# Kernel optimization log

Measured on AMD Instinct MI355X. Metric: run time of the kernel, lower is better.

## Reference

```python
import jax, jax.numpy as jnp
import numpy as np

N_EMBED = 1024
N_HEAD = 64  # head (value) dimension, per source: Linear(n_embed, n_head)
B = 8
C = 2048


def setup_inputs() -> dict:
    key = jax.random.key(0)
    k1, k2, k3, k4, k5 = jax.random.split(key, 5)
    bound = 1.0 / np.sqrt(N_EMBED)  # torch Linear default init range
    x = jax.random.normal(k1, (B, C, N_EMBED), dtype=jnp.float32)
    Wq = jax.random.uniform(k2, (N_EMBED, N_HEAD), dtype=jnp.float32, minval=-bound, maxval=bound)
    Wk = jax.random.uniform(k3, (N_EMBED, N_HEAD), dtype=jnp.float32, minval=-bound, maxval=bound)
    Wv = jax.random.uniform(k4, (N_EMBED, N_HEAD), dtype=jnp.float32, minval=-bound, maxval=bound)
    zero_mask = jax.random.randint(k5, (B, C), 0, 2) == 1
    return {"x": x, "Wq": Wq, "Wk": Wk, "Wv": Wv, "zero_mask": zero_mask}


def reference(x, Wq, Wk, Wv, zero_mask):
    # x: [B, C, n_embed]; zero_mask: [B, C] bool (zeroes whole query rows post-softmax)
    Bc, Cc, _ = x.shape
    q = x @ Wq  # [B, C, H]
    k = x @ Wk
    v = x @ Wv
    # NOTE: source scales by C**-0.5 (sequence length), not head_dim**-0.5
    scores = jnp.einsum('bqh,bkh->bqk', q, k) * (float(Cc) ** -0.5)  # [B, C, C]
    causal = jnp.tril(jnp.ones((Cc, Cc), dtype=bool))
    scores = jnp.where(causal[None], scores, -jnp.inf)
    a = jax.nn.softmax(scores, axis=-1)
    a = jnp.where(zero_mask[..., None], jnp.zeros((), dtype=a.dtype), a)  # post-softmax zero mask
    return a @ v  # [B, C, H]
```

## Files before the change

kernel.cpp:

```cpp
#include <hip/hip_runtime.h>
#include <math.h>


#define B_ 8
#define C_ 2048
#define E_ 1024
#define H_ 64
#define SCALE (0.02209708691207961f * 1.4426950408889634f)

typedef __attribute__((ext_vector_type(8))) short short8;
typedef __attribute__((ext_vector_type(4))) float floatx4;

union BF8 { short8 s8; unsigned int u[4]; };

static __device__ __forceinline__ unsigned int pack_bf2(float lo, float hi) {
    unsigned int a = __builtin_bit_cast(unsigned int, lo);
    unsigned int b = __builtin_bit_cast(unsigned int, hi);
    return (a >> 16) | (b & 0xFFFF0000u);
}
static __device__ __forceinline__ unsigned short f2bf(float f) {
    return (unsigned short)(__builtin_bit_cast(unsigned int, f) >> 16);
}
static __device__ __forceinline__ void load_lds16(const void* g, void* l) {
    __builtin_amdgcn_global_load_lds(
        (const __attribute__((address_space(1))) void*)g,
        (__attribute__((address_space(3))) void*)l, 16, 0, 0);
}

__global__ __launch_bounds__(256) void wcvt_kernel(
    const float* __restrict__ Wq, const float* __restrict__ Wk,
    const float* __restrict__ Wv, unsigned short* __restrict__ wt)
{
    __shared__ float lds[64][68];
    const int bid = (int)blockIdx.x;
    const int m = bid >> 4, kt = bid & 15, k0 = kt * 64;
    const float* W = (m == 0) ? Wq : (m == 1) ? Wk : Wv;
    const int t = (int)threadIdx.x;
#pragma unroll
    for (int j = 0; j < 4; j++) {
        int idx4 = j * 256 + t;
        int row = idx4 >> 4, c4 = idx4 & 15;
        float4 v = *(const float4*)(W + (size_t)(k0 + row) * 64 + c4 * 4);
        *(float4*)&lds[row][c4 * 4] = v;
    }
    __syncthreads();
#pragma unroll
    for (int j = 0; j < 2; j++) {
        int g = j * 256 + t;
        int n = g >> 3, kk = (g & 7) * 8;
        unsigned int o[4];
#pragma unroll
        for (int i = 0; i < 4; i++)
            o[i] = pack_bf2(lds[kk + 2 * i][n], lds[kk + 2 * i + 1][n]);
        *(uint4*)(wt + (size_t)(m * 64 + n) * 1024 + k0 + kk) =
            make_uint4(o[0], o[1], o[2], o[3]);
    }
}

__global__ __launch_bounds__(256, 2) void qkv_kernel(
    const float* __restrict__ X, const unsigned short* __restrict__ wt,
    unsigned short* __restrict__ qg, unsigned short* __restrict__ kg,
    unsigned short* __restrict__ vtile)
{
    __shared__ __align__(16) unsigned char smem[2 * 8192 + 2 * 24576];
    unsigned short* vstage = (unsigned short*)smem;

    const int t = (int)threadIdx.x;
    const int w = t >> 6, lane = t & 63;
    const int l15 = lane & 15, quad = lane >> 4;
    const int r0 = (int)blockIdx.x * 32;
    const int rbase = (w & 1) * 16;
    const int nloc0 = (w >> 1) * 96;

    const int wrow_off = lane >> 3, wgs = lane & 7;

    floatx4 acc[6];
#pragma unroll
    for (int j = 0; j < 6; j++) acc[j] = (floatx4){0.f, 0.f, 0.f, 0.f};

#define XBUF(q) (smem + (q) * 8192)
#define WBUF(q) (smem + 16384 + (q) * 24576)
#define STAGE_X(c, q) do {                                                   \
        _Pragma("unroll")                                                    \
        for (int j = 0; j < 2; j++) {                                        \
            const int gi = w * 128 + j * 64 + lane;                          \
            const int row = gi >> 4;                                         \
            const int g = (gi & 15) ^ (row & 15);                            \
            load_lds16(X + (size_t)(r0 + row) * E_ + (c) * 64 + g * 4,       \
                       XBUF(q) + (w * 128 + j * 64) * 16);                   \
        }                                                                    \
    } while (0)
#define STAGE_W(c, q) do {                                                   \
        _Pragma("unroll")                                                    \
        for (int j = 0; j < 6; j++) {                                        \
            const int region = w * 6 + j;                                    \
            const int nloc = region * 8 + wrow_off;                          \
            const int gsrc = wgs ^ (nloc & 7);                               \
            load_lds16(wt + (size_t)nloc * 1024 + (c) * 64 + gsrc * 8,       \
                       WBUF(q) + region * 1024);                             \
        }                                                                    \
    } while (0)

    STAGE_X(0, 0);
    STAGE_W(0, 0);

#pragma unroll
    for (int c = 0; c < 16; c++) {
        __syncthreads();
        if (c + 1 < 16) {
            STAGE_X(c + 1, (c + 1) & 1);
            STAGE_W(c + 1, (c + 1) & 1);
        }
        const float4* xc = (const float4*)XBUF(c & 1);
        const unsigned short* wc = (const unsigned short*)WBUF(c & 1);

#pragma unroll
        for (int ks = 0; ks < 2; ks++) {
            const int g0 = ks * 8 + quad * 2;
            const float4* xrow = xc + (rbase + l15) * 16;
            float4 f0 = xrow[g0 ^ l15];
            float4 f1 = xrow[(g0 + 1) ^ l15];
            BF8 a;
            a.u[0] = pack_bf2(f0.x, f0.y);
            a.u[1] = pack_bf2(f0.z, f0.w);
            a.u[2] = pack_bf2(f1.x, f1.y);
            a.u[3] = pack_bf2(f1.z, f1.w);
#pragma unroll
            for (int nt = 0; nt < 6; nt++) {
                const int nloc = nloc0 + nt * 16 + l15;
                const int slot = (ks * 4 + quad) ^ (nloc & 7);
                short8 bfr = *(const short8*)(wc + nloc * 64 + slot * 8);
                acc[nt] = __builtin_amdgcn_mfma_f32_16x16x32_bf16(
                    a.s8, bfr, acc[nt], 0, 0, 0);
            }
        }
    }
#undef STAGE_X
#undef STAGE_W
#undef XBUF
#undef WBUF

    const int bb = r0 >> 11;
    const int keybase = r0 & 2047;
    const int rowl0 = rbase + quad * 4;
    __syncthreads();
#pragma unroll
    for (int nt = 0; nt < 6; nt++) {
        const int n = nloc0 + nt * 16 + l15;
        if (n < 64) {
#pragma unroll
            for (int r = 0; r < 4; r++)
                qg[(size_t)(r0 + rowl0 + r) * 64 + n] = f2bf(acc[nt][r] * SCALE);
        } else if (n < 128) {
#pragma unroll
            for (int r = 0; r < 4; r++)
                kg[(size_t)(r0 + rowl0 + r) * 64 + (n - 64)] = f2bf(acc[nt][r]);
        } else {
            const int h = n - 128;
            *(unsigned int*)&vstage[h * 40 + rowl0] =
                pack_bf2(acc[nt][0], acc[nt][1]);
            *(unsigned int*)&vstage[h * 40 + rowl0 + 2] =
                pack_bf2(acc[nt][2], acc[nt][3]);
        }
    }
    __syncthreads();
    {
        const int h = t >> 2, part = t & 3;
        uint4 v = *(const uint4*)&vstage[h * 40 + part * 8];
        *(uint4*)(vtile + ((size_t)(bb * 32 + (keybase >> 6)) * 64 + h) * 64
                  + (keybase & 63) + part * 8) = v;
    }
}

__global__ __launch_bounds__(256, 3) void attn_kernel(
    const unsigned short* __restrict__ qg, const unsigned short* __restrict__ kg,
    const unsigned short* __restrict__ vtile, const int* __restrict__ zmask,
    float* __restrict__ opart, float* __restrict__ lpart,
    float* __restrict__ out)
{
    __shared__ unsigned short Klds[2][64 * 64];
    __shared__ unsigned short Vlds[2][64 * 64];
    __shared__ unsigned short Ps[64 * 88];

    const int t = (int)threadIdx.x;
    const int w = t >> 6, lane = t & 63;
    const int l15 = lane & 15, quad = lane >> 4;
    const int b = (int)blockIdx.x;
    const int qt = (int)blockIdx.y;
    const int z = (int)blockIdx.z;
    const int q0 = qt * 64;
    const int nkt = qt + 1;
    const int t0 = z * 8;
    const int t1 = (t0 + 8 < nkt) ? (t0 + 8) : nkt;
    if (t0 >= t1) return;
    const int ns = (nkt + 7) >> 3;

    const int qlo = q0 + w * 16;
    const int myrow = qlo + quad * 4;
    const int srow_off = lane >> 3, sgs = lane & 7;

    short8 qfr[2];
#pragma unroll
    for (int kc = 0; kc < 2; kc++)
        qfr[kc] = *(const short8*)(qg + ((size_t)b * C_ + qlo + l15) * 64
                                   + kc * 32 + quad * 8);

    floatx4 accO[4];
#pragma unroll
    for (int i = 0; i < 4; i++) accO[i] = (floatx4){0.f, 0.f, 0.f, 0.f};
    float lsum[4] = {0.f, 0.f, 0.f, 0.f};

#pragma unroll
    for (int j = 0; j < 2; j++) {
        const int region = w * 2 + j;
        const int row = region * 8 + srow_off;
        const int gsrc = sgs ^ (row & 7);
        load_lds16(kg + ((size_t)b * C_ + t0 * 64 + row) * 64 + gsrc * 8,
                   &Klds[0][region * 512]);
        load_lds16(vtile + (((size_t)b * 32 + t0) * 64 + row) * 64 + gsrc * 8,
                   &Vlds[0][region * 512]);
    }

    int buf = 0;
    for (int kt = t0; kt < t1; kt++) {
        __syncthreads();
        if (kt + 1 < t1) {
            const int k0n = (kt + 1) * 64;
#pragma unroll
            for (int j = 0; j < 2; j++) {
                const int region = w * 2 + j;
                const int row = region * 8 + srow_off;
                const int gsrc = sgs ^ (row & 7);
                load_lds16(kg + ((size_t)b * C_ + k0n + row) * 64 + gsrc * 8,
                           &Klds[buf ^ 1][region * 512]);
                load_lds16(vtile + (((size_t)b * 32 + kt + 1) * 64 + row) * 64 + gsrc * 8,
                           &Vlds[buf ^ 1][region * 512]);
            }
        }

        floatx4 s[4];
#pragma unroll
        for (int nt = 0; nt < 4; nt++) {
            const int row = nt * 16 + l15;
            short8 kf0 = *(const short8*)&Klds[buf][row * 64 + ((quad) ^ (row & 7)) * 8];
            short8 kf1 = *(const short8*)&Klds[buf][row * 64 + ((4 + quad) ^ (row & 7)) * 8];
            floatx4 zz = (floatx4){0.f, 0.f, 0.f, 0.f};
            zz = __builtin_amdgcn_mfma_f32_16x16x32_bf16(qfr[0], kf0, zz, 0, 0, 0);
            s[nt] = __builtin_amdgcn_mfma_f32_16x16x32_bf16(qfr[1], kf1, zz, 0, 0, 0);
        }
        float pr[4][4];
#pragma unroll
        for (int nt = 0; nt < 4; nt++)
#pragma unroll
            for (int r = 0; r < 4; r++)
                pr[nt][r] = __builtin_amdgcn_exp2f(s[nt][r]);
        if (kt == nkt - 1) {
            const int k0 = kt * 64;
#pragma unroll
            for (int nt = 0; nt < 4; nt++) {
                const int key = k0 + nt * 16 + l15;
#pragma unroll
                for (int r = 0; r < 4; r++)
                    if (key > myrow + r) pr[nt][r] = 0.f;
            }
        }
#pragma unroll
        for (int nt = 0; nt < 4; nt++)
#pragma unroll
            for (int r = 0; r < 4; r++) {
                lsum[r] += pr[nt][r];
                Ps[(w * 16 + quad * 4 + r) * 88 + nt * 16 + l15] = f2bf(pr[nt][r]);
            }
#pragma unroll
        for (int kc = 0; kc < 2; kc++) {
            short8 af = *(const short8*)&Ps[(w * 16 + l15) * 88 + kc * 32 + quad * 8];
#pragma unroll
            for (int nt = 0; nt < 4; nt++) {
                const int row = nt * 16 + l15;
                short8 vf = *(const short8*)&Vlds[buf][row * 64
                                + ((kc * 4 + quad) ^ (row & 7)) * 8];
                accO[nt] = __builtin_amdgcn_mfma_f32_16x16x32_bf16(
                    af, vf, accO[nt], 0, 0, 0);
            }
        }
        buf ^= 1;
    }

#pragma unroll
    for (int r = 0; r < 4; r++) {
        float v = lsum[r];
        v += __shfl_xor(v, 1);
        v += __shfl_xor(v, 2);
        v += __shfl_xor(v, 4);
        v += __shfl_xor(v, 8);
        lsum[r] = v;
    }

    if (ns == 1) {
        float inv[4];
#pragma unroll
        for (int r = 0; r < 4; r++) {
            int zm = zmask[b * C_ + myrow + r];
            inv[r] = zm ? 0.f : 1.0f / lsum[r];
        }
#pragma unroll
        for (int nt = 0; nt < 4; nt++)
#pragma unroll
            for (int r = 0; r < 4; r++)
                out[(size_t)(b * C_ + myrow + r) * 64 + nt * 16 + l15] =
                    accO[nt][r] * inv[r];
    } else {
        const int lrow = myrow - 512;
        float* ob = opart + ((size_t)(z * 8 + b) * 1536 + lrow) * 64;
#pragma unroll
        for (int nt = 0; nt < 4; nt++)
#pragma unroll
            for (int r = 0; r < 4; r++)
                ob[(size_t)r * 64 + nt * 16 + l15] = accO[nt][r];
        if (l15 == 0) {
#pragma unroll
            for (int r = 0; r < 4; r++)
                lpart[(size_t)(z * 8 + b) * 1536 + lrow + r] = lsum[r];
        }
    }
}

__global__ __launch_bounds__(256) void combine_kernel(
    const float* __restrict__ opart, const float* __restrict__ lpart,
    const int* __restrict__ zmask, float* __restrict__ out)
{
    const int b = (int)blockIdx.y;
    const int gid = (int)blockIdx.x * 256 + (int)threadIdx.x;
    const int lrow = gid >> 4;
    const int f4 = gid & 15;
    const int row = 512 + lrow;
    const int nkt = (row >> 6) + 1;
    const int ns = (nkt + 7) >> 3;

    float4 o = make_float4(0.f, 0.f, 0.f, 0.f);
    float l = 0.f;
    for (int zc = 0; zc < ns; zc++) {
        float4 p = *(const float4*)(opart
            + ((size_t)(zc * 8 + b) * 1536 + lrow) * 64 + f4 * 4);
        o.x += p.x; o.y += p.y; o.z += p.z; o.w += p.w;
        l += lpart[(size_t)(zc * 8 + b) * 1536 + lrow];
    }
    const float inv = zmask[b * C_ + row] ? 0.f : 1.0f / l;
    *(float4*)(out + (size_t)(b * C_ + row) * 64 + f4 * 4) =
        make_float4(o.x * inv, o.y * inv, o.z * inv, o.w * inv);
}

extern "C" void kernel_launch(void* const* d_in, const int* in_sizes, int n_in,
                              void* d_out, int out_size, void* d_ws, size_t ws_size,
                              hipStream_t stream) {
    const float* X  = (const float*)d_in[0];
    const float* Wq = (const float*)d_in[1];
    const float* Wk = (const float*)d_in[2];
    const float* Wv = (const float*)d_in[3];
    const int*   zm = (const int*)d_in[4];
    float* out = (float*)d_out;

    unsigned short* qg    = (unsigned short*)d_ws;
    unsigned short* kg    = qg    + (size_t)B_ * C_ * H_;
    unsigned short* vtile = kg    + (size_t)B_ * C_ * H_;
    unsigned short* wt    = vtile + (size_t)B_ * C_ * H_;
    float* opart = (float*)(wt + (size_t)192 * 1024);
    float* lpart = opart + (size_t)4 * 8 * 1536 * 64;

    wcvt_kernel<<<dim3(48), dim3(256), 0, stream>>>(Wq, Wk, Wv, wt);
    qkv_kernel<<<dim3(512), dim3(256), 0, stream>>>(X, wt, qg, kg, vtile);
    attn_kernel<<<dim3(B_, 32, 4), dim3(256), 0, stream>>>(
        qg, kg, vtile, zm, opart, lpart, out);
    combine_kernel<<<dim3(96, B_), dim3(256), 0, stream>>>(opart, lpart, zm, out);
}
```

Before: 132.3 us.

## Deepen K/V LDS pipeline to four buffers with explicit vmcnt waits and setprio

Replaces the double-buffered K/V staging with a 4-slot ring that prefetches two tiles ahead. Each iteration waits with explicit s_waitcnt vmcnt counts and a single raw barrier instead of a full __syncthreads at the top. MFMA sections are wrapped in s_setprio to favour matrix issue across waves. The aim is to hide global-to-LDS latency, but doubling K/V LDS lowers the launch-bounds occupancy hint from 3 to 2 blocks per CU. With only one barrier per iteration and a prefetch distance of 2 into 4 slots, a ring slot may be overwritten while slower waves still read it, a correctness risk that depends on how the waves skew.

```diff
diff --git a/kernel.cpp b/kernel.cpp
--- a/kernel.cpp
+++ b/kernel.cpp
@@ -172,14 +172,14 @@
     }
 }
 
-__global__ __launch_bounds__(256, 3) void attn_kernel(
+__global__ __launch_bounds__(256, 2) void attn_kernel(
     const unsigned short* __restrict__ qg, const unsigned short* __restrict__ kg,
     const unsigned short* __restrict__ vtile, const int* __restrict__ zmask,
     float* __restrict__ opart, float* __restrict__ lpart,
     float* __restrict__ out)
 {
-    __shared__ unsigned short Klds[2][64 * 64];
-    __shared__ unsigned short Vlds[2][64 * 64];
+    __shared__ unsigned short Klds[4][64 * 64];
+    __shared__ unsigned short Vlds[4][64 * 64];
     __shared__ unsigned short Ps[64 * 88];
 
     const int t = (int)threadIdx.x;
@@ -210,44 +210,47 @@
     for (int i = 0; i < 4; i++) accO[i] = (floatx4){0.f, 0.f, 0.f, 0.f};
     float lsum[4] = {0.f, 0.f, 0.f, 0.f};
 
-#pragma unroll
-    for (int j = 0; j < 2; j++) {
-        const int region = w * 2 + j;
-        const int row = region * 8 + srow_off;
-        const int gsrc = sgs ^ (row & 7);
-        load_lds16(kg + ((size_t)b * C_ + t0 * 64 + row) * 64 + gsrc * 8,
-                   &Klds[0][region * 512]);
-        load_lds16(vtile + (((size_t)b * 32 + t0) * 64 + row) * 64 + gsrc * 8,
-                   &Vlds[0][region * 512]);
-    }
-
-    int buf = 0;
-    for (int kt = t0; kt < t1; kt++) {
-        __syncthreads();
-        if (kt + 1 < t1) {
-            const int k0n = (kt + 1) * 64;
-#pragma unroll
-            for (int j = 0; j < 2; j++) {
-                const int region = w * 2 + j;
-                const int row = region * 8 + srow_off;
-                const int gsrc = sgs ^ (row & 7);
-                load_lds16(kg + ((size_t)b * C_ + k0n + row) * 64 + gsrc * 8,
-                           &Klds[buf ^ 1][region * 512]);
-                load_lds16(vtile + (((size_t)b * 32 + kt + 1) * 64 + row) * 64 + gsrc * 8,
-                           &Vlds[buf ^ 1][region * 512]);
-            }
-        }
+#define STAGE(tile, bi) do {                                                  \
+        const int k0s = (tile) * 64;                                          \
+        _Pragma("unroll")                                                     \
+        for (int j = 0; j < 2; j++) {                                         \
+            const int region = w * 2 + j;                                     \
+            const int row = region * 8 + srow_off;                            \
+            const int gsrc = sgs ^ (row & 7);                                 \
+            load_lds16(kg + ((size_t)b * C_ + k0s + row) * 64 + gsrc * 8,     \
+                       &Klds[bi][region * 512]);                              \
+            load_lds16(vtile + (((size_t)b * 32 + (tile)) * 64 + row) * 64    \
+                           + gsrc * 8,                                        \
+                       &Vlds[bi][region * 512]);                              \
+        }                                                                     \
+    } while (0)
+
+    const int NT = t1 - t0;
+    STAGE(t0, 0);
+    if (NT > 1) STAGE(t0 + 1, 1);
+
+    for (int i = 0; i < NT; i++) {
+        const int kt = t0 + i;
+        if (i + 2 < NT) STAGE(kt + 2, (i + 2) & 3);
+        if (i + 2 < NT)      asm volatile("s_waitcnt vmcnt(8)" ::: "memory");
+        else if (i + 1 < NT) asm volatile("s_waitcnt vmcnt(4)" ::: "memory");
+        else                 asm volatile("s_waitcnt vmcnt(0)" ::: "memory");
+        __builtin_amdgcn_s_barrier();
+        __builtin_amdgcn_sched_barrier(0);
+        const int bi = i & 3;
 
         floatx4 s[4];
+        __builtin_amdgcn_s_setprio(1);
 #pragma unroll
         for (int nt = 0; nt < 4; nt++) {
             const int row = nt * 16 + l15;
-            short8 kf0 = *(const short8*)&Klds[buf][row * 64 + ((quad) ^ (row & 7)) * 8];
-            short8 kf1 = *(const short8*)&Klds[buf][row * 64 + ((4 + quad) ^ (row & 7)) * 8];
+            short8 kf0 = *(const short8*)&Klds[bi][row * 64 + ((quad) ^ (row & 7)) * 8];
+            short8 kf1 = *(const short8*)&Klds[bi][row * 64 + ((4 + quad) ^ (row & 7)) * 8];
             floatx4 zz = (floatx4){0.f, 0.f, 0.f, 0.f};
             zz = __builtin_amdgcn_mfma_f32_16x16x32_bf16(qfr[0], kf0, zz, 0, 0, 0);
             s[nt] = __builtin_amdgcn_mfma_f32_16x16x32_bf16(qfr[1], kf1, zz, 0, 0, 0);
         }
+        __builtin_amdgcn_s_setprio(0);
         float pr[4][4];
 #pragma unroll
         for (int nt = 0; nt < 4; nt++)
@@ -271,20 +274,22 @@
                 lsum[r] += pr[nt][r];
                 Ps[(w * 16 + quad * 4 + r) * 88 + nt * 16 + l15] = f2bf(pr[nt][r]);
             }
+        __builtin_amdgcn_s_setprio(1);
 #pragma unroll
         for (int kc = 0; kc < 2; kc++) {
             short8 af = *(const short8*)&Ps[(w * 16 + l15) * 88 + kc * 32 + quad * 8];
 #pragma unroll
             for (int nt = 0; nt < 4; nt++) {
                 const int row = nt * 16 + l15;
-                short8 vf = *(const short8*)&Vlds[buf][row * 64
+                short8 vf = *(const short8*)&Vlds[bi][row * 64
                                 + ((kc * 4 + quad) ^ (row & 7)) * 8];
                 accO[nt] = __builtin_amdgcn_mfma_f32_16x16x32_bf16(
                     af, vf, accO[nt], 0, 0, 0);
             }
         }
-        buf ^= 1;
-    }
+        __builtin_amdgcn_s_setprio(0);
+    }
+#undef STAGE
 
 #pragma unroll
     for (int r = 0; r < 4; r++) {
```

After: 136.8 us. 1.03x slower.

## Pre-swizzle weights into MFMA fragment order and load directly into registers

Applied to the files above, without the earlier changes.

The weight conversion kernel now writes bf16 weights in per-lane MFMA fragment order, so the QKV projection loads B fragments straight from global memory into registers, double-buffered, instead of staging them through LDS. This removes 48KB of LDS per block and the LDS reads, at the cost of 24 short8 registers of weight fragments per thread. The attention kernel also replaces the padded P scratch buffer with an XOR-swizzled 64-wide layout, shrinking LDS, and raises its launch-bounds occupancy hint from 3 to 4 blocks, which may increase register pressure.

```diff
diff --git a/kernel.cpp b/kernel.cpp
--- a/kernel.cpp
+++ b/kernel.cpp
@@ -29,7 +29,7 @@
 
 __global__ __launch_bounds__(256) void wcvt_kernel(
     const float* __restrict__ Wq, const float* __restrict__ Wk,
-    const float* __restrict__ Wv, unsigned short* __restrict__ wt)
+    const float* __restrict__ Wv, unsigned short* __restrict__ wtf)
 {
     __shared__ float lds[64][68];
     const int bid = (int)blockIdx.x;
@@ -45,24 +45,29 @@
     }
     __syncthreads();
 #pragma unroll
-    for (int j = 0; j < 2; j++) {
-        int g = j * 256 + t;
-        int n = g >> 3, kk = (g & 7) * 8;
+    for (int h = 0; h < 2; h++) {
+        int fl = h * 256 + t;
+        int ntl = fl >> 7;
+        int ks = (fl >> 6) & 1;
+        int lane = fl & 63;
+        int n = ntl * 16 + (lane & 15);
+        int kb = ks * 32 + (lane >> 4) * 8;
         unsigned int o[4];
 #pragma unroll
         for (int i = 0; i < 4; i++)
-            o[i] = pack_bf2(lds[kk + 2 * i][n], lds[kk + 2 * i + 1][n]);
-        *(uint4*)(wt + (size_t)(m * 64 + n) * 1024 + k0 + kk) =
+            o[i] = pack_bf2(lds[kb + 2 * i][n], lds[kb + 2 * i + 1][n]);
+        size_t frag = ((size_t)kt * 12 + (m * 4 + ntl)) * 2 + ks;
+        *(uint4*)(wtf + frag * 512 + lane * 8) =
             make_uint4(o[0], o[1], o[2], o[3]);
     }
 }
 
 __global__ __launch_bounds__(256, 2) void qkv_kernel(
-    const float* __restrict__ X, const unsigned short* __restrict__ wt,
+    const float* __restrict__ X, const unsigned short* __restrict__ wtf,
     unsigned short* __restrict__ qg, unsigned short* __restrict__ kg,
     unsigned short* __restrict__ vtile)
 {
-    __shared__ __align__(16) unsigned char smem[2 * 8192 + 2 * 24576];
+    __shared__ __align__(16) unsigned char smem[2 * 8192];
     unsigned short* vstage = (unsigned short*)smem;
 
     const int t = (int)threadIdx.x;
@@ -70,16 +75,15 @@
     const int l15 = lane & 15, quad = lane >> 4;
     const int r0 = (int)blockIdx.x * 32;
     const int rbase = (w & 1) * 16;
-    const int nloc0 = (w >> 1) * 96;
-
-    const int wrow_off = lane >> 3, wgs = lane & 7;
+    const int ntg0 = (w >> 1) * 6;
 
     floatx4 acc[6];
 #pragma unroll
     for (int j = 0; j < 6; j++) acc[j] = (floatx4){0.f, 0.f, 0.f, 0.f};
 
+    short8 wf[2][6][2];
+
 #define XBUF(q) (smem + (q) * 8192)
-#define WBUF(q) (smem + 16384 + (q) * 24576)
 #define STAGE_X(c, q) do {                                                   \
         _Pragma("unroll")                                                    \
         for (int j = 0; j < 2; j++) {                                        \
@@ -90,29 +94,27 @@
                        XBUF(q) + (w * 128 + j * 64) * 16);                   \
         }                                                                    \
     } while (0)
-#define STAGE_W(c, q) do {                                                   \
+#define LOADW(c, p) do {                                                     \
         _Pragma("unroll")                                                    \
-        for (int j = 0; j < 6; j++) {                                        \
-            const int region = w * 6 + j;                                    \
-            const int nloc = region * 8 + wrow_off;                          \
-            const int gsrc = wgs ^ (nloc & 7);                               \
-            load_lds16(wt + (size_t)nloc * 1024 + (c) * 64 + gsrc * 8,       \
-                       WBUF(q) + region * 1024);                             \
-        }                                                                    \
+        for (int nt = 0; nt < 6; nt++)                                       \
+            _Pragma("unroll")                                                \
+            for (int ks = 0; ks < 2; ks++)                                   \
+                wf[p][nt][ks] = *(const short8*)(wtf +                       \
+                    ((size_t)(((c) * 12 + ntg0 + nt) * 2 + ks)) * 512        \
+                    + lane * 8);                                             \
     } while (0)
 
     STAGE_X(0, 0);
-    STAGE_W(0, 0);
+    LOADW(0, 0);
 
 #pragma unroll
     for (int c = 0; c < 16; c++) {
         __syncthreads();
         if (c + 1 < 16) {
             STAGE_X(c + 1, (c + 1) & 1);
-            STAGE_W(c + 1, (c + 1) & 1);
+            LOADW(c + 1, (c + 1) & 1);
         }
         const float4* xc = (const float4*)XBUF(c & 1);
-        const unsigned short* wc = (const unsigned short*)WBUF(c & 1);
 
 #pragma unroll
         for (int ks = 0; ks < 2; ks++) {
@@ -126,19 +128,14 @@
             a.u[2] = pack_bf2(f1.x, f1.y);
             a.u[3] = pack_bf2(f1.z, f1.w);
 #pragma unroll
-            for (int nt = 0; nt < 6; nt++) {
-                const int nloc = nloc0 + nt * 16 + l15;
-                const int slot = (ks * 4 + quad) ^ (nloc & 7);
-                short8 bfr = *(const short8*)(wc + nloc * 64 + slot * 8);
+            for (int nt = 0; nt < 6; nt++)
                 acc[nt] = __builtin_amdgcn_mfma_f32_16x16x32_bf16(
-                    a.s8, bfr, acc[nt], 0, 0, 0);
-            }
+                    a.s8, wf[c & 1][nt][ks], acc[nt], 0, 0, 0);
         }
     }
 #undef STAGE_X
-#undef STAGE_W
+#undef LOADW
 #undef XBUF
-#undef WBUF
 
     const int bb = r0 >> 11;
     const int keybase = r0 & 2047;
@@ -146,7 +143,7 @@
     __syncthreads();
 #pragma unroll
     for (int nt = 0; nt < 6; nt++) {
-        const int n = nloc0 + nt * 16 + l15;
+        const int n = ntg0 * 16 + nt * 16 + l15;
         if (n < 64) {
 #pragma unroll
             for (int r = 0; r < 4; r++)
@@ -172,7 +169,7 @@
     }
 }
 
-__global__ __launch_bounds__(256, 3) void attn_kernel(
+__global__ __launch_bounds__(256, 4) void attn_kernel(
     const unsigned short* __restrict__ qg, const unsigned short* __restrict__ kg,
     const unsigned short* __restrict__ vtile, const int* __restrict__ zmask,
     float* __restrict__ opart, float* __restrict__ lpart,
@@ -180,7 +177,7 @@
 {
     __shared__ unsigned short Klds[2][64 * 64];
     __shared__ unsigned short Vlds[2][64 * 64];
-    __shared__ unsigned short Ps[64 * 88];
+    __shared__ unsigned short Ps[64 * 64];
 
     const int t = (int)threadIdx.x;
     const int w = t >> 6, lane = t & 63;
@@ -269,11 +266,15 @@
 #pragma unroll
             for (int r = 0; r < 4; r++) {
                 lsum[r] += pr[nt][r];
-                Ps[(w * 16 + quad * 4 + r) * 88 + nt * 16 + l15] = f2bf(pr[nt][r]);
+                const int prow = w * 16 + quad * 4 + r;
+                const int slot = (nt * 2 + (l15 >> 3)) ^ (prow & 7);
+                Ps[prow * 64 + slot * 8 + (l15 & 7)] = f2bf(pr[nt][r]);
             }
 #pragma unroll
         for (int kc = 0; kc < 2; kc++) {
-            short8 af = *(const short8*)&Ps[(w * 16 + l15) * 88 + kc * 32 + quad * 8];
+            const int arow = w * 16 + l15;
+            short8 af = *(const short8*)&Ps[arow * 64
+                            + (((kc * 4 + quad) ^ (l15 & 7)) * 8)];
 #pragma unroll
             for (int nt = 0; nt < 4; nt++) {
                 const int row = nt * 16 + l15;
@@ -363,12 +364,12 @@
     unsigned short* qg    = (unsigned short*)d_ws;
     unsigned short* kg    = qg    + (size_t)B_ * C_ * H_;
     unsigned short* vtile = kg    + (size_t)B_ * C_ * H_;
-    unsigned short* wt    = vtile + (size_t)B_ * C_ * H_;
-    float* opart = (float*)(wt + (size_t)192 * 1024);
+    unsigned short* wtf   = vtile + (size_t)B_ * C_ * H_;
+    float* opart = (float*)(wtf + (size_t)192 * 1024);
     float* lpart = opart + (size_t)4 * 8 * 1536 * 64;
 
-    wcvt_kernel<<<dim3(48), dim3(256), 0, stream>>>(Wq, Wk, Wv, wt);
-    qkv_kernel<<<dim3(512), dim3(256), 0, stream>>>(X, wt, qg, kg, vtile);
+    wcvt_kernel<<<dim3(48), dim3(256), 0, stream>>>(Wq, Wk, Wv, wtf);
+    qkv_kernel<<<dim3(512), dim3(256), 0, stream>>>(X, wtf, qg, kg, vtile);
     attn_kernel<<<dim3(B_, 32, 4), dim3(256), 0, stream>>>(
         qg, kg, vtile, zm, opart, lpart, out);
     combine_kernel<<<dim3(96, B_), dim3(256), 0, stream>>>(opart, lpart, zm, out);
```

Measured after the change: 141.6 us. 7.1% more time.

## Enlarge QKV tile to 64 rows and stage X as bf16 through registers

Applied to the files above, without the earlier changes.

The QKV projection kernel now uses 512-thread blocks that each cover 64 rows instead of 32. Each W chunk loaded into LDS is therefore reused across twice as many rows, which halves total W traffic. X is no longer copied to LDS as fp32 with direct global-to-LDS loads. It is loaded into registers, converted to bf16 once, and written to a swizzled bf16 LDS buffer, so the repeated per-MFMA conversion goes away. The register-staged prefetch ties global load latency to the compute loop, and the grid shrinks to 256 blocks, which may underfill the GPU.

```diff
diff --git a/kernel.cpp b/kernel.cpp
--- a/kernel.cpp
+++ b/kernel.cpp
@@ -10,8 +10,6 @@
 
 typedef __attribute__((ext_vector_type(8))) short short8;
 typedef __attribute__((ext_vector_type(4))) float floatx4;
-
-union BF8 { short8 s8; unsigned int u[4]; };
 
 static __device__ __forceinline__ unsigned int pack_bf2(float lo, float hi) {
     unsigned int a = __builtin_bit_cast(unsigned int, lo);
@@ -57,7 +55,7 @@
     }
 }
 
-__global__ __launch_bounds__(256, 2) void qkv_kernel(
+__global__ __launch_bounds__(512, 2) void qkv_kernel(
     const float* __restrict__ X, const unsigned short* __restrict__ wt,
     unsigned short* __restrict__ qg, unsigned short* __restrict__ kg,
     unsigned short* __restrict__ vtile)
@@ -68,107 +66,108 @@
     const int t = (int)threadIdx.x;
     const int w = t >> 6, lane = t & 63;
     const int l15 = lane & 15, quad = lane >> 4;
-    const int r0 = (int)blockIdx.x * 32;
-    const int rbase = (w & 1) * 16;
-    const int nloc0 = (w >> 1) * 96;
+    const int r0 = (int)blockIdx.x * 64;
+    const int rbase = (w & 3) * 16;
+    const int nloc0 = (w >> 2) * 96;
 
     const int wrow_off = lane >> 3, wgs = lane & 7;
 
+    const int xr = t >> 3;
+    const int xg = t & 7;
+    const int xslot = xg ^ (xr & 7);
+    const float* xsrc = X + (size_t)(r0 + xr) * E_ + xg * 8;
+
     floatx4 acc[6];
 #pragma unroll
     for (int j = 0; j < 6; j++) acc[j] = (floatx4){0.f, 0.f, 0.f, 0.f};
 
-#define XBUF(q) (smem + (q) * 8192)
-#define WBUF(q) (smem + 16384 + (q) * 24576)
-#define STAGE_X(c, q) do {                                                   \
-        _Pragma("unroll")                                                    \
-        for (int j = 0; j < 2; j++) {                                        \
-            const int gi = w * 128 + j * 64 + lane;                          \
-            const int row = gi >> 4;                                         \
-            const int g = (gi & 15) ^ (row & 15);                            \
-            load_lds16(X + (size_t)(r0 + row) * E_ + (c) * 64 + g * 4,       \
-                       XBUF(q) + (w * 128 + j * 64) * 16);                   \
-        }                                                                    \
+    float4 xa0, xa1;
+
+#define XBUF(q) ((unsigned short*)(smem + (q) * 8192))
+#define WBUF(q) ((unsigned short*)(smem + 16384 + (q) * 24576))
+#define LOADX(c) do {                                                        \
+        xa0 = *(const float4*)(xsrc + (size_t)(c) * 64);                     \
+        xa1 = *(const float4*)(xsrc + (size_t)(c) * 64 + 4);                 \
+    } while (0)
+#define WRITEX(q) do {                                                       \
+        uint4 o = make_uint4(pack_bf2(xa0.x, xa0.y), pack_bf2(xa0.z, xa0.w), \
+                             pack_bf2(xa1.x, xa1.y), pack_bf2(xa1.z, xa1.w));\
+        *(uint4*)(XBUF(q) + xr * 64 + xslot * 8) = o;                        \
     } while (0)
 #define STAGE_W(c, q) do {                                                   \
         _Pragma("unroll")                                                    \
-        for (int j = 0; j < 6; j++) {                                        \
-            const int region = w * 6 + j;                                    \
+        for (int j = 0; j < 3; j++) {                                        \
+            const int region = w * 3 + j;                                    \
             const int nloc = region * 8 + wrow_off;                          \
             const int gsrc = wgs ^ (nloc & 7);                               \
             load_lds16(wt + (size_t)nloc * 1024 + (c) * 64 + gsrc * 8,       \
-                       WBUF(q) + region * 1024);                             \
+                       (unsigned char*)WBUF(q) + region * 1024);             \
         }                                                                    \
     } while (0)
 
-    STAGE_X(0, 0);
+    LOADX(0);
     STAGE_W(0, 0);
+    WRITEX(0);
+    __syncthreads();
 
 #pragma unroll
     for (int c = 0; c < 16; c++) {
-        __syncthreads();
         if (c + 1 < 16) {
-            STAGE_X(c + 1, (c + 1) & 1);
+            LOADX(c + 1);
             STAGE_W(c + 1, (c + 1) & 1);
         }
-        const float4* xc = (const float4*)XBUF(c & 1);
-        const unsigned short* wc = (const unsigned short*)WBUF(c & 1);
-
+        const unsigned short* xc = XBUF(c & 1);
+        const unsigned short* wc = WBUF(c & 1);
 #pragma unroll
         for (int ks = 0; ks < 2; ks++) {
-            const int g0 = ks * 8 + quad * 2;
-            const float4* xrow = xc + (rbase + l15) * 16;
-            float4 f0 = xrow[g0 ^ l15];
-            float4 f1 = xrow[(g0 + 1) ^ l15];
-            BF8 a;
-            a.u[0] = pack_bf2(f0.x, f0.y);
-            a.u[1] = pack_bf2(f0.z, f0.w);
-            a.u[2] = pack_bf2(f1.x, f1.y);
-            a.u[3] = pack_bf2(f1.z, f1.w);
+            const int arow = rbase + l15;
+            short8 af = *(const short8*)(xc + arow * 64
+                            + (((ks * 4 + quad) ^ (arow & 7)) * 8));
 #pragma unroll
             for (int nt = 0; nt < 6; nt++) {
                 const int nloc = nloc0 + nt * 16 + l15;
                 const int slot = (ks * 4 + quad) ^ (nloc & 7);
                 short8 bfr = *(const short8*)(wc + nloc * 64 + slot * 8);
                 acc[nt] = __builtin_amdgcn_mfma_f32_16x16x32_bf16(
-                    a.s8, bfr, acc[nt], 0, 0, 0);
-            }
-        }
-    }
-#undef STAGE_X
+                    af, bfr, acc[nt], 0, 0, 0);
+            }
+        }
+        if (c + 1 < 16) WRITEX((c + 1) & 1);
+        __syncthreads();
+    }
+#undef LOADX
+#undef WRITEX
 #undef STAGE_W
 #undef XBUF
 #undef WBUF
 
     const int bb = r0 >> 11;
-    const int keybase = r0 & 2047;
-    const int rowl0 = rbase + quad * 4;
-    __syncthreads();
+    const int kb = (r0 >> 6) & 31;
+    const int keyl = rbase + quad * 4;
 #pragma unroll
     for (int nt = 0; nt < 6; nt++) {
         const int n = nloc0 + nt * 16 + l15;
         if (n < 64) {
 #pragma unroll
             for (int r = 0; r < 4; r++)
-                qg[(size_t)(r0 + rowl0 + r) * 64 + n] = f2bf(acc[nt][r] * SCALE);
+                qg[(size_t)(r0 + keyl + r) * 64 + n] = f2bf(acc[nt][r] * SCALE);
         } else if (n < 128) {
 #pragma unroll
             for (int r = 0; r < 4; r++)
-                kg[(size_t)(r0 + rowl0 + r) * 64 + (n - 64)] = f2bf(acc[nt][r]);
+                kg[(size_t)(r0 + keyl + r) * 64 + (n - 64)] = f2bf(acc[nt][r]);
         } else {
             const int h = n - 128;
-            *(unsigned int*)&vstage[h * 40 + rowl0] =
+            *(unsigned int*)&vstage[h * 72 + keyl] =
                 pack_bf2(acc[nt][0], acc[nt][1]);
-            *(unsigned int*)&vstage[h * 40 + rowl0 + 2] =
+            *(unsigned int*)&vstage[h * 72 + keyl + 2] =
                 pack_bf2(acc[nt][2], acc[nt][3]);
         }
     }
     __syncthreads();
     {
-        const int h = t >> 2, part = t & 3;
-        uint4 v = *(const uint4*)&vstage[h * 40 + part * 8];
-        *(uint4*)(vtile + ((size_t)(bb * 32 + (keybase >> 6)) * 64 + h) * 64
-                  + (keybase & 63) + part * 8) = v;
+        const int h = t >> 3, part = t & 7;
+        uint4 v = *(const uint4*)&vstage[h * 72 + part * 8];
+        *(uint4*)(vtile + ((size_t)(bb * 32 + kb) * 64 + h) * 64 + part * 8) = v;
     }
 }
 
@@ -368,7 +367,7 @@
     float* lpart = opart + (size_t)4 * 8 * 1536 * 64;
 
     wcvt_kernel<<<dim3(48), dim3(256), 0, stream>>>(Wq, Wk, Wv, wt);
-    qkv_kernel<<<dim3(512), dim3(256), 0, stream>>>(X, wt, qg, kg, vtile);
+    qkv_kernel<<<dim3(256), dim3(512), 0, stream>>>(X, wt, qg, kg, vtile);
     attn_kernel<<<dim3(B_, 32, 4), dim3(256), 0, stream>>>(
         qg, kg, vtile, zm, opart, lpart, out);
     combine_kernel<<<dim3(96, B_), dim3(256), 0, stream>>>(opart, lpart, zm, out);
```

Measured after the change: 132.5 us. Within noise of the previous version (+0.1%).
